# Kernel optimization log

Hardware: AMD Instinct MI355X
Metric: run time of the kernel (lower is better)

Reference implementation:

```python
import jax, jax.numpy as jnp
import numpy as np

EPS = 1e-12
B, DIN, T, DH = 32, 512, 4096, 500


def setup_inputs() -> dict:
    key = jax.random.key(0)
    k1, k2, k3 = jax.random.split(key, 3)
    x = jax.random.normal(k1, (B, DIN, T), dtype=jnp.float32)
    weight1 = jax.random.normal(k2, (DH, DIN), dtype=jnp.float32) * (1.0 / np.sqrt(DIN))
    weight2 = jax.random.normal(k3, (1, DH), dtype=jnp.float32) * (1.0 / np.sqrt(DH))
    return {"x": x, "weight1": weight1, "weight2": weight2, "dim": 2}


def reference(x, weight1, weight2, dim):
    # x: (B, din, T)
    h = jnp.swapaxes(x, 1, 2)                      # (B, T, din)
    a = jax.nn.relu(jnp.einsum('btd,hd->bth', h, weight1))  # (B, T, dh)
    scores = jnp.einsum('bth,oh->bto', a, weight2)           # (B, T, 1)
    attn = jax.nn.softmax(scores, axis=1)                    # softmax over time
    mean = jnp.einsum('bdt,bto->bdo', x, attn)               # (B, din, 1)
    variance = jnp.mean((x - mean) ** 2, axis=dim)           # (B, din) unweighted
    mean_s = jnp.squeeze(mean, axis=dim)                     # (B, din)
    mask = (variance <= EPS).astype(variance.dtype)
    variance = (1.0 - mask) * variance + mask * EPS
    stddev = jnp.sqrt(variance)
    return jnp.concatenate((mean_s, stddev), axis=-1)        # (B, 2*din)
```

## Files before the change

### kernel.cpp

```cpp
#include <hip/hip_runtime.h>
#include <hip/hip_bf16.h>

#define NB 32
#define DIN 512
#define TT 4096
#define DH 500
#define DHP 512
#define EPSV 1e-12f
#define BM 64
#define LDA 520

typedef short short8 __attribute__((ext_vector_type(8)));
typedef float f32x16 __attribute__((ext_vector_type(16)));
typedef float f32x4 __attribute__((ext_vector_type(4)));

__device__ inline unsigned short f2bf(float f) {
    unsigned int u = __builtin_bit_cast(unsigned int, f);
    unsigned int r = (u + 0x7fffu + ((u >> 16) & 1u)) >> 16;
    return (unsigned short)r;
}

__global__ void prep_kernel(const float* __restrict__ w1, const float* __restrict__ w2,
                            unsigned short* __restrict__ w1b, float* __restrict__ w2f) {
    int idx = blockIdx.x * blockDim.x + threadIdx.x;
    if (idx < DHP * DIN) {
        const int j    = idx & 7;
        const int lane = (idx >> 3) & 63;
        const int ks   = (idx >> 9) & 31;
        const int hb   = idx >> 14;
        const int h = hb * 32 + (lane & 31);
        const int d = ks * 16 + (lane >> 5) * 8 + j;
        float v = (h < DH) ? w1[h * DIN + d] : 0.f;
        w1b[idx] = f2bf(v);
        if (idx < DHP) w2f[idx] = (idx < DH) ? w2[idx] : 0.f;
    }
}

__launch_bounds__(512, 4)
__global__ void scores_kernel(const float* __restrict__ x,
                              const unsigned short* __restrict__ w1b,
                              const float* __restrict__ w2f,
                              float* __restrict__ scores) {
    __shared__ unsigned short A_lds[BM][LDA];
    __shared__ float score_lds[BM];

    const int tid = threadIdx.x;
    const int b = blockIdx.x >> 6;
    const int t0 = (blockIdx.x & 63) * BM;

    if (tid < BM) score_lds[tid] = 0.f;

    {
        const int ts = tid & 63;
        const int dg = tid >> 6;
        const float* xb = x + (size_t)b * DIN * TT + t0 + ts;
        #pragma unroll
        for (int oct = 0; oct < 8; ++oct) {
            const int d0 = dg * 64 + oct * 8;
            short8 pk;
            #pragma unroll
            for (int j = 0; j < 8; ++j)
                pk[j] = (short)f2bf(xb[(size_t)(d0 + j) * TT]);
            *reinterpret_cast<short8*>(&A_lds[ts][d0]) = pk;
        }
    }
    __syncthreads();

    const int w = tid >> 6;
    const int lane = tid & 63;
    const int lane31 = lane & 31;
    const int khalf = lane >> 5;
    const int hrow0 = w * 64;

    f32x16 acc00, acc01, acc10, acc11;
    #pragma unroll
    for (int g = 0; g < 16; ++g) { acc00[g] = 0.f; acc01[g] = 0.f; acc10[g] = 0.f; acc11[g] = 0.f; }

    const unsigned short* base0 = w1b + (size_t)w * 32768 + (size_t)lane * 8;
    const unsigned short* base1 = base0 + 16384;
    const unsigned short* Bp0 = &A_lds[lane31][khalf * 8];
    const unsigned short* Bp1 = &A_lds[32 + lane31][khalf * 8];

    #pragma unroll 4
    for (int ks = 0; ks < 32; ++ks) {
        short8 a0 = *reinterpret_cast<const short8*>(base0 + ks * 512);
        short8 a1 = *reinterpret_cast<const short8*>(base1 + ks * 512);
        short8 b0 = *reinterpret_cast<const short8*>(Bp0 + ks * 16);
        short8 b1 = *reinterpret_cast<const short8*>(Bp1 + ks * 16);
        acc00 = __builtin_amdgcn_mfma_f32_32x32x16_bf16(a0, b0, acc00, 0, 0, 0);
        acc01 = __builtin_amdgcn_mfma_f32_32x32x16_bf16(a0, b1, acc01, 0, 0, 0);
        acc10 = __builtin_amdgcn_mfma_f32_32x32x16_bf16(a1, b0, acc10, 0, 0, 0);
        acc11 = __builtin_amdgcn_mfma_f32_32x32x16_bf16(a1, b1, acc11, 0, 0, 0);
    }

    float s0 = 0.f, s1 = 0.f;
    #pragma unroll
    for (int g = 0; g < 16; ++g) {
        const int rp = (g & 3) + 8 * (g >> 2) + 4 * khalf;
        const float w20 = w2f[hrow0 + rp];
        const float w21 = w2f[hrow0 + 32 + rp];
        s0 += fmaxf(acc00[g], 0.f) * w20 + fmaxf(acc10[g], 0.f) * w21;
        s1 += fmaxf(acc01[g], 0.f) * w20 + fmaxf(acc11[g], 0.f) * w21;
    }
    s0 += __shfl_xor(s0, 32, 64);
    s1 += __shfl_xor(s1, 32, 64);
    if (khalf == 0) {
        atomicAdd(&score_lds[lane31], s0);
        atomicAdd(&score_lds[32 + lane31], s1);
    }
    __syncthreads();
    if (tid < BM) scores[(size_t)b * TT + t0 + tid] = score_lds[tid];
}

__global__ void softmax_kernel(const float* __restrict__ scores, float* __restrict__ attn) {
    __shared__ float red[8];
    const int b = blockIdx.x;
    const int tid = threadIdx.x;
    const float* srow = scores + (size_t)b * TT;
    float v[16];
    float mx = -1e30f;
    #pragma unroll
    for (int j = 0; j < 16; ++j) { v[j] = srow[tid + 256 * j]; mx = fmaxf(mx, v[j]); }
    #pragma unroll
    for (int m = 1; m <= 32; m <<= 1) mx = fmaxf(mx, __shfl_xor(mx, m, 64));
    if ((tid & 63) == 0) red[tid >> 6] = mx;
    __syncthreads();
    mx = fmaxf(fmaxf(red[0], red[1]), fmaxf(red[2], red[3]));
    float sum = 0.f;
    #pragma unroll
    for (int j = 0; j < 16; ++j) { v[j] = __expf(v[j] - mx); sum += v[j]; }
    #pragma unroll
    for (int m = 1; m <= 32; m <<= 1) sum += __shfl_xor(sum, m, 64);
    if ((tid & 63) == 0) red[4 + (tid >> 6)] = sum;
    __syncthreads();
    sum = red[4] + red[5] + red[6] + red[7];
    const float inv = 1.f / sum;
    float* arow = attn + (size_t)b * TT;
    #pragma unroll
    for (int j = 0; j < 16; ++j) arow[tid + 256 * j] = v[j] * inv;
}

__global__ void stats_kernel(const float* __restrict__ x, const float* __restrict__ attn,
                             float* __restrict__ out) {
    const int w = threadIdx.x >> 6;
    const int lane = threadIdx.x & 63;
    const int row = blockIdx.x * 4 + w;
    const int b = row >> 9;
    const int d = row & 511;
    const float* xr = x + (size_t)row * TT;
    const float* ar = attn + (size_t)b * TT;
    float sx = 0.f, sx2 = 0.f, sxw = 0.f;
    #pragma unroll 4
    for (int i = 0; i < 16; ++i) {
        int t = (i * 64 + lane) * 4;
        f32x4 xv = *reinterpret_cast<const f32x4*>(xr + t);
        f32x4 av = *reinterpret_cast<const f32x4*>(ar + t);
        #pragma unroll
        for (int j = 0; j < 4; ++j) {
            float xx = xv[j];
            sx += xx; sx2 += xx * xx; sxw += xx * av[j];
        }
    }
    #pragma unroll
    for (int m = 1; m <= 32; m <<= 1) {
        sx  += __shfl_xor(sx, m, 64);
        sx2 += __shfl_xor(sx2, m, 64);
        sxw += __shfl_xor(sxw, m, 64);
    }
    if (lane == 0) {
        const float mean = sxw;
        const float ex = sx * (1.f / TT);
        const float ex2 = sx2 * (1.f / TT);
        float var = ex2 - 2.f * mean * ex + mean * mean;
        if (var <= EPSV) var = EPSV;
        out[(size_t)b * 1024 + d] = mean;
        out[(size_t)b * 1024 + 512 + d] = sqrtf(var);
    }
}

extern "C" void kernel_launch(void* const* d_in, const int* in_sizes, int n_in,
                              void* d_out, int out_size, void* d_ws, size_t ws_size,
                              hipStream_t stream) {
    const float* x  = (const float*)d_in[0];
    const float* w1 = (const float*)d_in[1];
    const float* w2 = (const float*)d_in[2];
    float* out = (float*)d_out;

    char* ws = (char*)d_ws;
    unsigned short* w1b = (unsigned short*)ws;
    float* w2f   = (float*)(ws + DHP * DIN * 2);
    float* scores = (float*)(ws + DHP * DIN * 2 + 2048);
    float* attn   = scores + NB * TT;

    prep_kernel<<<(DHP * DIN + 255) / 256, 256, 0, stream>>>(w1, w2, w1b, w2f);
    scores_kernel<<<NB * (TT / BM), 512, 0, stream>>>(x, w1b, w2f, scores);
    softmax_kernel<<<NB, 256, 0, stream>>>(scores, attn);
    stats_kernel<<<NB * DIN / 4, 256, 0, stream>>>(x, attn, out);
}
```

Baseline: 135.5 us.

## Fuse tile softmax and statistics into scores kernel with online-softmax combine

The scores kernel now computes a per-tile local softmax (max and sum of exponentials). It also accumulates per-channel sum, sum of squares and exp-weighted sums from the bf16 x tile already held in LDS, writing these as partials. A small combine kernel then merges the partials across tiles with online-softmax rescaling to produce mean and stddev. This removes the separate softmax and stats kernels and the second full read of x from global memory. In exchange, the statistics are computed from bf16-rounded x rather than fp32, and the combine step runs on only one block per batch.

```diff
diff --git a/kernel.cpp b/kernel.cpp
--- a/kernel.cpp
+++ b/kernel.cpp
@@ -9,6 +9,7 @@
 #define EPSV 1e-12f
 #define BM 64
 #define LDA 520
+#define NTILES (TT / BM)
 
 typedef short short8 __attribute__((ext_vector_type(8)));
 typedef float f32x16 __attribute__((ext_vector_type(16)));
@@ -18,6 +19,10 @@
     unsigned int u = __builtin_bit_cast(unsigned int, f);
     unsigned int r = (u + 0x7fffu + ((u >> 16) & 1u)) >> 16;
     return (unsigned short)r;
+}
+__device__ inline float bf2f(unsigned short h) {
+    unsigned int u = ((unsigned int)h) << 16;
+    return __builtin_bit_cast(float, u);
 }
 
 __global__ void prep_kernel(const float* __restrict__ w1, const float* __restrict__ w2,
@@ -37,18 +42,19 @@
 }
 
 __launch_bounds__(512, 4)
-__global__ void scores_kernel(const float* __restrict__ x,
-                              const unsigned short* __restrict__ w1b,
-                              const float* __restrict__ w2f,
-                              float* __restrict__ scores) {
+__global__ void scores_fused(const float* __restrict__ x,
+                             const unsigned short* __restrict__ w1b,
+                             const float* __restrict__ w2f,
+                             float* __restrict__ pm, float* __restrict__ pz,
+                             float* __restrict__ pswx, float* __restrict__ psx,
+                             float* __restrict__ psx2) {
     __shared__ unsigned short A_lds[BM][LDA];
-    __shared__ float score_lds[BM];
+    __shared__ float score_p[8][BM];
+    __shared__ float w_lds[BM];
 
     const int tid = threadIdx.x;
     const int b = blockIdx.x >> 6;
     const int t0 = (blockIdx.x & 63) * BM;
-
-    if (tid < BM) score_lds[tid] = 0.f;
 
     {
         const int ts = tid & 63;
@@ -105,77 +111,73 @@
     s0 += __shfl_xor(s0, 32, 64);
     s1 += __shfl_xor(s1, 32, 64);
     if (khalf == 0) {
-        atomicAdd(&score_lds[lane31], s0);
-        atomicAdd(&score_lds[32 + lane31], s1);
-    }
-    __syncthreads();
-    if (tid < BM) scores[(size_t)b * TT + t0 + tid] = score_lds[tid];
-}
-
-__global__ void softmax_kernel(const float* __restrict__ scores, float* __restrict__ attn) {
-    __shared__ float red[8];
+        score_p[w][lane31] = s0;
+        score_p[w][32 + lane31] = s1;
+    }
+    __syncthreads();
+
+    if (tid < BM) {
+        float s = 0.f;
+        #pragma unroll
+        for (int ww = 0; ww < 8; ++ww) s += score_p[ww][tid];
+        float m = s;
+        #pragma unroll
+        for (int k = 1; k <= 32; k <<= 1) m = fmaxf(m, __shfl_xor(m, k, 64));
+        float e = __expf(s - m);
+        float Z = e;
+        #pragma unroll
+        for (int k = 1; k <= 32; k <<= 1) Z += __shfl_xor(Z, k, 64);
+        w_lds[tid] = e;
+        if (tid == 0) { pm[blockIdx.x] = m; pz[blockIdx.x] = Z; }
+    }
+    __syncthreads();
+
+    {
+        const int d = tid;
+        float sx = 0.f, sx2 = 0.f, swx = 0.f;
+        #pragma unroll 8
+        for (int t = 0; t < BM; ++t) {
+            const float xv = bf2f(A_lds[t][d]);
+            const float wv = w_lds[t];
+            sx += xv; sx2 += xv * xv; swx += wv * xv;
+        }
+        const size_t o = (size_t)blockIdx.x * DHP + d;
+        psx[o] = sx; psx2[o] = sx2; pswx[o] = swx;
+    }
+}
+
+__global__ void combine_kernel(const float* __restrict__ pm, const float* __restrict__ pz,
+                               const float* __restrict__ pswx, const float* __restrict__ psx,
+                               const float* __restrict__ psx2, float* __restrict__ out) {
+    __shared__ float sm[NTILES], sz[NTILES];
     const int b = blockIdx.x;
     const int tid = threadIdx.x;
-    const float* srow = scores + (size_t)b * TT;
-    float v[16];
-    float mx = -1e30f;
-    #pragma unroll
-    for (int j = 0; j < 16; ++j) { v[j] = srow[tid + 256 * j]; mx = fmaxf(mx, v[j]); }
-    #pragma unroll
-    for (int m = 1; m <= 32; m <<= 1) mx = fmaxf(mx, __shfl_xor(mx, m, 64));
-    if ((tid & 63) == 0) red[tid >> 6] = mx;
-    __syncthreads();
-    mx = fmaxf(fmaxf(red[0], red[1]), fmaxf(red[2], red[3]));
-    float sum = 0.f;
-    #pragma unroll
-    for (int j = 0; j < 16; ++j) { v[j] = __expf(v[j] - mx); sum += v[j]; }
-    #pragma unroll
-    for (int m = 1; m <= 32; m <<= 1) sum += __shfl_xor(sum, m, 64);
-    if ((tid & 63) == 0) red[4 + (tid >> 6)] = sum;
-    __syncthreads();
-    sum = red[4] + red[5] + red[6] + red[7];
-    const float inv = 1.f / sum;
-    float* arow = attn + (size_t)b * TT;
-    #pragma unroll
-    for (int j = 0; j < 16; ++j) arow[tid + 256 * j] = v[j] * inv;
-}
-
-__global__ void stats_kernel(const float* __restrict__ x, const float* __restrict__ attn,
-                             float* __restrict__ out) {
-    const int w = threadIdx.x >> 6;
-    const int lane = threadIdx.x & 63;
-    const int row = blockIdx.x * 4 + w;
-    const int b = row >> 9;
-    const int d = row & 511;
-    const float* xr = x + (size_t)row * TT;
-    const float* ar = attn + (size_t)b * TT;
-    float sx = 0.f, sx2 = 0.f, sxw = 0.f;
+    if (tid < NTILES) { sm[tid] = pm[b * NTILES + tid]; sz[tid] = pz[b * NTILES + tid]; }
+    __syncthreads();
+
+    float mg = -1e30f;
+    #pragma unroll 8
+    for (int i = 0; i < NTILES; ++i) mg = fmaxf(mg, sm[i]);
+    float denom = 0.f;
+    #pragma unroll 8
+    for (int i = 0; i < NTILES; ++i) denom += sz[i] * __expf(sm[i] - mg);
+
+    float num = 0.f, sx = 0.f, sx2 = 0.f;
     #pragma unroll 4
-    for (int i = 0; i < 16; ++i) {
-        int t = (i * 64 + lane) * 4;
-        f32x4 xv = *reinterpret_cast<const f32x4*>(xr + t);
-        f32x4 av = *reinterpret_cast<const f32x4*>(ar + t);
-        #pragma unroll
-        for (int j = 0; j < 4; ++j) {
-            float xx = xv[j];
-            sx += xx; sx2 += xx * xx; sxw += xx * av[j];
-        }
-    }
-    #pragma unroll
-    for (int m = 1; m <= 32; m <<= 1) {
-        sx  += __shfl_xor(sx, m, 64);
-        sx2 += __shfl_xor(sx2, m, 64);
-        sxw += __shfl_xor(sxw, m, 64);
-    }
-    if (lane == 0) {
-        const float mean = sxw;
-        const float ex = sx * (1.f / TT);
-        const float ex2 = sx2 * (1.f / TT);
-        float var = ex2 - 2.f * mean * ex + mean * mean;
-        if (var <= EPSV) var = EPSV;
-        out[(size_t)b * 1024 + d] = mean;
-        out[(size_t)b * 1024 + 512 + d] = sqrtf(var);
-    }
+    for (int i = 0; i < NTILES; ++i) {
+        const size_t o = ((size_t)(b * NTILES + i)) * DHP + tid;
+        const float f = __expf(sm[i] - mg);
+        num += f * pswx[o];
+        sx  += psx[o];
+        sx2 += psx2[o];
+    }
+    const float mean = num / denom;
+    const float ex  = sx  * (1.f / TT);
+    const float ex2 = sx2 * (1.f / TT);
+    float var = ex2 - 2.f * mean * ex + mean * mean;
+    if (var <= EPSV) var = EPSV;
+    out[(size_t)b * 1024 + tid] = mean;
+    out[(size_t)b * 1024 + 512 + tid] = sqrtf(var);
 }
 
 extern "C" void kernel_launch(void* const* d_in, const int* in_sizes, int n_in,
@@ -188,12 +190,14 @@
 
     char* ws = (char*)d_ws;
     unsigned short* w1b = (unsigned short*)ws;
-    float* w2f   = (float*)(ws + DHP * DIN * 2);
-    float* scores = (float*)(ws + DHP * DIN * 2 + 2048);
-    float* attn   = scores + NB * TT;
+    float* w2f  = (float*)(ws + 524288);
+    float* pm   = (float*)(ws + 526336);
+    float* pz   = (float*)(ws + 534528);
+    float* pswx = (float*)(ws + 542720);
+    float* psx  = pswx + (size_t)NB * NTILES * DHP;
+    float* psx2 = psx  + (size_t)NB * NTILES * DHP;
 
     prep_kernel<<<(DHP * DIN + 255) / 256, 256, 0, stream>>>(w1, w2, w1b, w2f);
-    scores_kernel<<<NB * (TT / BM), 512, 0, stream>>>(x, w1b, w2f, scores);
-    softmax_kernel<<<NB, 256, 0, stream>>>(scores, attn);
-    stats_kernel<<<NB * DIN / 4, 256, 0, stream>>>(x, attn, out);
-}
+    scores_fused<<<NB * NTILES, 512, 0, stream>>>(x, w1b, w2f, pm, pz, pswx, psx, psx2);
+    combine_kernel<<<NB, 512, 0, stream>>>(pm, pz, pswx, psx, psx2, out);
+}
```

After: 124.2 us. 8.3% less time.
